# Performance work log

Measured on AMD Instinct MI355X. Metric: run time of the kernel, lower is better.

## Reference

```python
import jax, jax.numpy as jnp
import numpy as np

B, N, DIM = 8, 8192, 256
HEADS, LOCAL_HEADS, WINDOW = 8, 1, 64
HD = DIM // HEADS  # 32
MLP_HIDDEN = 1024
EPS = 1e-5


def layer_norm(x, g, b):
    mu = jnp.mean(x, axis=-1, keepdims=True)
    var = jnp.var(x, axis=-1, keepdims=True)
    return (x - mu) * jax.lax.rsqrt(var + EPS) * g + b


def look_around(t, pad_value=0.0):
    # t: (b, nw, w, ...); concat windows [i-1, i, i+1] -> (b, nw, 3w, ...)
    nw = t.shape[1]
    pads = [(0, 0), (1, 1)] + [(0, 0)] * (t.ndim - 2)
    p = jnp.pad(t, pads, constant_values=pad_value)
    return jnp.concatenate([p[:, i:i + nw] for i in range(3)], axis=2)


def local_attn(q, k, v):
    # lucidrains LocalAttention, causal=False, look_backward=look_forward=1
    # q,k,v: (b_merged, n, d)
    b, n, d = q.shape
    nw = n // WINDOW
    scale = d ** -0.5
    bq = q.reshape(b, nw, WINDOW, d) * scale
    bk = look_around(k.reshape(b, nw, WINDOW, d))  # (b, nw, 3w, d)
    bv = look_around(v.reshape(b, nw, WINDOW, d))
    ticker = jnp.arange(n).reshape(1, nw, WINDOW)
    bq_k = look_around(ticker, pad_value=-1)       # (1, nw, 3w)
    pad_mask = (bq_k == -1)[:, :, None, :]         # (1, nw, 1, 3w)
    dots = jnp.einsum('bnie,bnje->bnij', bq, bk)   # (b, nw, w, 3w)
    dots = jnp.where(pad_mask, -1e9, dots)
    attn = jax.nn.softmax(dots, axis=-1)
    out = jnp.einsum('bnij,bnje->bnie', attn, bv)
    return out.reshape(b, n, d)


def linear_attn(q, k, v):
    # q,k,v: (b, h, n, d)
    d = q.shape[-1]
    qs = jax.nn.softmax(q, axis=-1) * d ** -0.5
    ks = jax.nn.softmax(k, axis=-2)
    ctx = jnp.einsum('bhnd,bhne->bhde', ks, v)     # (b, h, d, d) tiny
    return jnp.einsum('bhnd,bhde->bhne', qs, ctx)


def setup_inputs() -> dict:
    key = jax.random.key(0)
    ks = jax.random.split(key, 8)
    s = 0.02
    return {
        'x': jax.random.normal(ks[0], (B, N, DIM), jnp.float32),
        'norm1_g': jnp.ones((DIM,), jnp.float32),
        'norm1_b': jnp.zeros((DIM,), jnp.float32),
        'Wq': jax.random.normal(ks[1], (DIM, DIM), jnp.float32) * s,
        'Wkv': jax.random.normal(ks[2], (DIM, DIM), jnp.float32) * s,
        'Wproj': jax.random.normal(ks[3], (DIM, DIM), jnp.float32) * s,
        'bproj': jnp.zeros((DIM,), jnp.float32),
        'norm2_g': jnp.ones((DIM,), jnp.float32),
        'norm2_b': jnp.zeros((DIM,), jnp.float32),
        'W1': jax.random.normal(ks[4], (MLP_HIDDEN, DIM), jnp.float32) * s,
        'b1': jnp.zeros((MLP_HIDDEN,), jnp.float32),
        'W2': jax.random.normal(ks[5], (DIM, MLP_HIDDEN), jnp.float32) * s,
        'b2': jnp.zeros((DIM,), jnp.float32),
    }


def reference(x, norm1_g, norm1_b, Wq, Wkv, Wproj, bproj, norm2_g, norm2_b, W1, b1, W2, b2):
    b, n, c = x.shape
    h = layer_norm(x, norm1_g, norm1_b)
    q = h @ Wq.T
    kv = h @ Wkv.T  # k and v share the same projection in the original code
    split_heads = lambda t: t.reshape(b, n, HEADS, HD).transpose(0, 2, 1, 3)
    q, k, v = split_heads(q), split_heads(kv), split_heads(kv)
    lq, gq = q[:, :LOCAL_HEADS], q[:, LOCAL_HEADS:]
    lk, gk = k[:, :LOCAL_HEADS], k[:, LOCAL_HEADS:]
    lv, gv = v[:, :LOCAL_HEADS], v[:, LOCAL_HEADS:]
    lout = local_attn(lq.reshape(b * LOCAL_HEADS, n, HD),
                      lk.reshape(b * LOCAL_HEADS, n, HD),
                      lv.reshape(b * LOCAL_HEADS, n, HD)).reshape(b, LOCAL_HEADS, n, HD)
    gout = linear_attn(gq, gk, gv)
    attn = jnp.concatenate([lout, gout], axis=1)   # (b, H, n, hd)
    y = attn.transpose(0, 2, 1, 3).reshape(b, n, c) @ Wproj.T + bproj
    x = x + y
    h2 = layer_norm(x, norm2_g, norm2_b)
    m = jax.nn.gelu(h2 @ W1.T + b1, approximate=False) @ W2.T + b2
    return x + m
```

## Files before the change

### kernel.cpp

```cpp
#include <hip/hip_runtime.h>
#include <hip/hip_bf16.h>

typedef __bf16 bf16;
typedef __bf16 bf16x8 __attribute__((ext_vector_type(8)));
typedef float f32x4 __attribute__((ext_vector_type(4)));

__device__ __forceinline__ void gld16(const void* g, void* l) {
  __builtin_amdgcn_global_load_lds((const __attribute__((address_space(1))) void*)g,
                                   (__attribute__((address_space(3))) void*)l, 16, 0, 0);
}

__global__ void cvt_weights(const float* __restrict__ wq, const float* __restrict__ wkv,
                            const float* __restrict__ wp, const float* __restrict__ w1,
                            const float* __restrict__ w2,
                            bf16* __restrict__ wqkv, bf16* __restrict__ wpb,
                            bf16* __restrict__ w1b, bf16* __restrict__ w2b) {
  int i = blockIdx.x * 256 + threadIdx.x;
  if (i < 65536) wqkv[i] = (bf16)wq[i];
  else if (i < 131072) wqkv[i] = (bf16)wkv[i - 65536];
  else if (i < 196608) wpb[i - 131072] = (bf16)wp[i - 131072];
  else if (i < 458752) w1b[i - 196608] = (bf16)w1[i - 196608];
  else if (i < 720896) w2b[i - 458752] = (bf16)w2[i - 458752];
}

__launch_bounds__(256)
__global__ void ln_kernel(const float* __restrict__ x, const float* __restrict__ g,
                          const float* __restrict__ b, bf16* __restrict__ out) {
  const int row = blockIdx.x * 4 + (threadIdx.x >> 6);
  const int lane = threadIdx.x & 63;
  const float4 v = ((const float4*)(x + (long)row * 256))[lane];
  float s = v.x + v.y + v.z + v.w;
#pragma unroll
  for (int o = 1; o < 64; o <<= 1) s += __shfl_xor(s, o);
  const float mu = s * (1.f / 256.f);
  const float dx = v.x - mu, dy = v.y - mu, dz = v.z - mu, dw = v.w - mu;
  float q = dx * dx + dy * dy + dz * dz + dw * dw;
#pragma unroll
  for (int o = 1; o < 64; o <<= 1) q += __shfl_xor(q, o);
  const float rstd = rsqrtf(q * (1.f / 256.f) + 1e-5f);
  const float4 gg = ((const float4*)g)[lane];
  const float4 bb = ((const float4*)b)[lane];
  union { bf16 h[4]; uint2 u; } pk;
  pk.h[0] = (bf16)(dx * rstd * gg.x + bb.x);
  pk.h[1] = (bf16)(dy * rstd * gg.y + bb.y);
  pk.h[2] = (bf16)(dz * rstd * gg.z + bb.z);
  pk.h[3] = (bf16)(dw * rstd * gg.w + bb.w);
  *(uint2*)(out + (long)row * 256 + lane * 4) = pk.u;
}

template <int EPI, int NCG, int NCHUNK, int THREADS, int MSPLIT>
__launch_bounds__(THREADS, 4)
__global__ void gemm_pb(const bf16* __restrict__ A, const bf16* __restrict__ Bw,
                        void* C, const float* __restrict__ bias,
                        const float* res, int ldC) {
  constexpr int WAVES = THREADS / 64;
  constexpr int WR = 2;
  constexpr int WC = WAVES / WR;
  constexpr int FN = 2;
  constexpr int FM = 64 / WR / 16;
  constexpr int COLS = WC * FN * 16;
  constexpr int KK = NCHUNK * 128;
  constexpr int ITER = 64 * 128 * 2 / (THREADS * 16);
  constexpr int TILES = 65536 / MSPLIT / 64;
  constexpr int CHB = 64 * 128 * 2;
  constexpr int BSZ = (EPI == 1) ? 64 * COLS * 4 : 64 * COLS * 2;
  constexpr int NST = (EPI == 1) ? 12 : 2;
  constexpr int NBLK = NCG * MSPLIT;
  __shared__ char smem[3 * CHB + BSZ];
  const int tid = threadIdx.x;
  const int w = tid >> 6, lane = tid & 63;
  const int l15 = lane & 15, l4 = lane >> 4;
  const int wrow = w & (WR - 1), wcol = w / WR;
  const int bid = blockIdx.x;
  const int slot = (bid & 7) * (NBLK / 8) + (bid >> 3);
  const int cg = slot % NCG;
  const long strip0 = (long)(slot / NCG) * (65536 / MSPLIT);

  const bf16* Bl = Bw + (long)(cg * COLS + wcol * FN * 16 + l15) * KK + l4 * 8;
  bf16x8 Breg[NCHUNK][4][FN];
#pragma unroll
  for (int c = 0; c < NCHUNK; ++c)
#pragma unroll
    for (int kl = 0; kl < 4; ++kl)
#pragma unroll
      for (int fn = 0; fn < FN; ++fn)
        Breg[c][kl][fn] = *(const bf16x8*)(Bl + (long)fn * 16 * KK + c * 128 + kl * 32);

  float bias_r[FN];
  if constexpr (EPI == 2) {
#pragma unroll
    for (int fn = 0; fn < FN; ++fn)
      bias_r[fn] = bias[cg * COLS + wcol * FN * 16 + fn * 16 + l15];
  }
  asm volatile("" ::: "memory");

  auto stage = [&](int m, int c, int buf) {
#pragma unroll
    for (int it = 0; it < ITER; ++it) {
      const int p = it * (THREADS * 16) + tid * 16;
      const int row = p >> 8;
      const int colb = (p & 255) ^ ((row & 7) << 4);
      gld16((const char*)A + ((strip0 + m * 64 + row) * KK + c * 128) * 2 + colb,
            smem + buf * CHB + it * (THREADS * 16) + w * 1024);
    }
  };

  f32x4 acc[FM][FN] = {};
  stage(0, 0, 0);
  stage(0, 1, 1);

  for (int m = 0; m < TILES; ++m) {
#pragma unroll
    for (int c = 0; c < NCHUNK; ++c) {
      const int s = m * NCHUNK + c;
      if (m == 0 || c >= 2) {
        asm volatile("s_waitcnt vmcnt(%0)" ::"i"(ITER) : "memory");
      } else {
        asm volatile("s_waitcnt vmcnt(%0)" ::"i"(ITER + NST) : "memory");
      }
      __syncthreads();
      {
        int c2 = c + 2, m2 = m;
        if (c2 >= NCHUNK) { c2 -= NCHUNK; ++m2; }
        if (m2 < TILES) stage(m2, c2, (s + 2) % 3);
      }
      const char* Ab = smem + (s % 3) * CHB;
#pragma unroll
      for (int kl = 0; kl < 4; ++kl) {
        bf16x8 af[FM];
#pragma unroll
        for (int fm = 0; fm < FM; ++fm) {
          const int arow = wrow * (64 / WR) + fm * 16 + l15;
          af[fm] = *(const bf16x8*)(Ab + arow * 256 + ((kl * 64 + l4 * 16) ^ ((l15 & 7) << 4)));
        }
#pragma unroll
        for (int fm = 0; fm < FM; ++fm)
#pragma unroll
          for (int fn = 0; fn < FN; ++fn)
            acc[fm][fn] = __builtin_amdgcn_mfma_f32_16x16x32_bf16(af[fm], Breg[c][kl][fn],
                                                                  acc[fm][fn], 0, 0, 0);
      }
      if (c == NCHUNK - 1) {
        if constexpr (EPI == 1) {
          float* fb = (float*)(smem + 3 * CHB);
#pragma unroll
          for (int fm = 0; fm < FM; ++fm)
#pragma unroll
            for (int fn = 0; fn < FN; ++fn)
#pragma unroll
              for (int r = 0; r < 4; ++r)
                fb[(wrow * (64 / WR) + fm * 16 + l4 * 4 + r) * COLS +
                   wcol * FN * 16 + fn * 16 + l15] = acc[fm][fn][r];
          __syncthreads();
#pragma unroll
          for (int it = 0; it < 64 * COLS * 4 / (THREADS * 16); ++it) {
            const int off = it * (THREADS * 16) + tid * 16;
            const int row = off / (COLS * 4);
            const int colb = off % (COLS * 4);
            const long gb = ((strip0 + m * 64 + row) * ldC + cg * COLS) * 4 + colb;
            float4 v = *(const float4*)(smem + 3 * CHB + off);
            const float4 rr = *(const float4*)((const char*)res + gb);
            const float4 bv = *(const float4*)((const char*)bias + cg * COLS * 4 + colb);
            v.x += rr.x + bv.x; v.y += rr.y + bv.y;
            v.z += rr.z + bv.z; v.w += rr.w + bv.w;
            *(float4*)((char*)C + gb) = v;
          }
        } else {
          bf16* bb = (bf16*)(smem + 3 * CHB);
#pragma unroll
          for (int fm = 0; fm < FM; ++fm)
#pragma unroll
            for (int fn = 0; fn < FN; ++fn)
#pragma unroll
              for (int r = 0; r < 4; ++r) {
                float v = acc[fm][fn][r];
                if constexpr (EPI == 2) {
                  v += bias_r[fn];
                  v = 0.5f * v * (1.f + erff(v * 0.70710678118654752f));
                }
                bb[(wrow * (64 / WR) + fm * 16 + l4 * 4 + r) * COLS +
                   wcol * FN * 16 + fn * 16 + l15] = (bf16)v;
              }
          __syncthreads();
#pragma unroll
          for (int it = 0; it < 64 * COLS * 2 / (THREADS * 16); ++it) {
            const int off = it * (THREADS * 16) + tid * 16;
            const int row = off / (COLS * 2);
            const int colb = off % (COLS * 2);
            *(uint4*)((char*)C + ((strip0 + m * 64 + row) * ldC + cg * COLS) * 2 + colb) =
                *(const uint4*)(smem + 3 * CHB + off);
          }
        }
#pragma unroll
        for (int fm = 0; fm < FM; ++fm)
#pragma unroll
          for (int fn = 0; fn < FN; ++fn)
            acc[fm][fn] = f32x4{0.f, 0.f, 0.f, 0.f};
      }
    }
  }
}

__launch_bounds__(256, 3)
__global__ void gemm_mlp2(const bf16* __restrict__ A, const bf16* __restrict__ Bw,
                          float* __restrict__ C, const float* __restrict__ bias) {
  constexpr int TILES = 2, NCHUNK = 8, ITER = 4, CHB = 64 * 128 * 2;
  __shared__ char smem[3 * CHB];
  const int tid = threadIdx.x;
  const int w = tid >> 6, lane = tid & 63;
  const int l15 = lane & 15, l4 = lane >> 4;
  const int bid = blockIdx.x;
  const int slot = (bid & 7) * 128 + (bid >> 3);
  const int cg = slot & 1;
  const long strip0 = (long)(slot >> 1) * 128;
  const bf16* Bl = Bw + (long)(cg * 128 + w * 32 + l15) * 1024 + l4 * 8;
  const float bias0 = bias[cg * 128 + w * 32 + l15];
  const float bias1 = bias[cg * 128 + w * 32 + 16 + l15];

  auto stage = [&](int m, int c, int buf) {
#pragma unroll
    for (int it = 0; it < ITER; ++it) {
      const int p = it * 4096 + tid * 16;
      const int row = p >> 8;
      const int colb = (p & 255) ^ ((row & 7) << 4);
      gld16((const char*)A + ((strip0 + m * 64 + row) * 1024 + c * 128) * 2 + colb,
            smem + buf * CHB + it * 4096 + w * 1024);
    }
  };
  auto loadB = [&](int c, bf16x8 (&Bn)[2][4]) {
#pragma unroll
    for (int fn = 0; fn < 2; ++fn)
#pragma unroll
      for (int kl = 0; kl < 4; ++kl)
        Bn[fn][kl] = *(const bf16x8*)(Bl + (long)fn * 16 * 1024 + c * 128 + kl * 32);
  };

  bf16x8 B0[2][4], B1[2][4];
  f32x4 acc[4][2] = {};
  stage(0, 0, 0);
  stage(0, 1, 1);
  loadB(0, B0);

  auto body = [&](int m, int c, bf16x8 (&Bu)[2][4], bf16x8 (&Bn)[2][4]) {
    const int s = m * NCHUNK + c;
    if (s == 0)
      asm volatile("s_waitcnt vmcnt(12)" ::: "memory");
    else if (s == TILES * NCHUNK - 1)
      asm volatile("s_waitcnt vmcnt(16)" ::: "memory");
    else
      asm volatile("s_waitcnt vmcnt(20)" ::: "memory");
    __syncthreads();
    {
      int c2 = c + 2, m2 = m;
      if (c2 >= NCHUNK) { c2 -= NCHUNK; ++m2; }
      if (m2 < TILES) stage(m2, c2, (s + 2) % 3);
    }
    loadB((c + 1) & 7, Bn);
    const char* Ab = smem + (s % 3) * CHB;
#pragma unroll
    for (int kl = 0; kl < 4; ++kl) {
      bf16x8 af[4];
#pragma unroll
      for (int fm = 0; fm < 4; ++fm)
        af[fm] = *(const bf16x8*)(Ab + (fm * 16 + l15) * 256 + ((kl * 64 + l4 * 16) ^ ((l15 & 7) << 4)));
#pragma unroll
      for (int fm = 0; fm < 4; ++fm) {
        acc[fm][0] = __builtin_amdgcn_mfma_f32_16x16x32_bf16(af[fm], Bu[0][kl], acc[fm][0], 0, 0, 0);
        acc[fm][1] = __builtin_amdgcn_mfma_f32_16x16x32_bf16(af[fm], Bu[1][kl], acc[fm][1], 0, 0, 0);
      }
    }
    if (c == NCHUNK - 1) {
#pragma unroll
      for (int fm = 0; fm < 4; ++fm)
#pragma unroll
        for (int r = 0; r < 4; ++r) {
          const long row = strip0 + m * 64 + fm * 16 + l4 * 4 + r;
          const long i0 = row * 256 + cg * 128 + w * 32 + l15;
          C[i0]      = acc[fm][0][r] + bias0 + C[i0];
          C[i0 + 16] = acc[fm][1][r] + bias1 + C[i0 + 16];
          acc[fm][0][r] = 0.f;
          acc[fm][1][r] = 0.f;
        }
      asm volatile("s_waitcnt vmcnt(12)" ::: "memory");
    }
  };

  for (int m = 0; m < TILES; ++m) {
#pragma unroll
    for (int cp = 0; cp < NCHUNK; cp += 2) {
      body(m, cp, B0, B1);
      body(m, cp + 1, B1, B0);
    }
  }
}

__launch_bounds__(256)
__global__ void lattn_kernel(const bf16* __restrict__ qkv, bf16* __restrict__ attn) {
  const int j = blockIdx.x, b = blockIdx.y;
  const int tid = threadIdx.x, w = tid >> 6, lane = tid & 63;
  __shared__ bf16 Qs[64 * 40];
  __shared__ bf16 Ks[192 * 40];
  __shared__ bf16 Kt[32 * 200];
  __shared__ bf16 Ps[4][16 * 200];
  const float scale = 0.17677669529663687f;
  const long base = (long)b * 8192 + (long)j * 64;
  for (int i = tid; i < 64 * 32; i += 256) {
    const int r = i >> 5, d = i & 31;
    Qs[r * 40 + d] = (bf16)((float)qkv[(base + r) * 512 + d] * scale);
  }
  for (int i = tid; i < 192 * 32; i += 256) {
    const int c = i >> 5, d = i & 31;
    const long tc = (long)j * 64 - 64 + c;
    float kv = 0.f;
    if (tc >= 0 && tc < 8192) kv = (float)qkv[((long)b * 8192 + tc) * 512 + 256 + d];
    const bf16 kb = (bf16)kv;
    Ks[c * 40 + d] = kb;
    Kt[d * 200 + c] = kb;
  }
  __syncthreads();
  const int l15 = lane & 15, l4 = lane >> 4;
  const bf16x8 aq = *(const bf16x8*)(Qs + (w * 16 + l15) * 40 + l4 * 8);
  const f32x4 zz = {0.f, 0.f, 0.f, 0.f};
  f32x4 S[12];
#pragma unroll
  for (int fn = 0; fn < 12; ++fn) {
    const bf16x8 bk = *(const bf16x8*)(Ks + (fn * 16 + l15) * 40 + l4 * 8);
    S[fn] = __builtin_amdgcn_mfma_f32_16x16x32_bf16(aq, bk, zz, 0, 0, 0);
  }
#pragma unroll
  for (int fn = 0; fn < 12; ++fn) {
    const long tc = (long)j * 64 - 64 + fn * 16 + l15;
    if (tc < 0 || tc >= 8192) { S[fn][0] = -1e9f; S[fn][1] = -1e9f; S[fn][2] = -1e9f; S[fn][3] = -1e9f; }
  }
  float sinv[4];
#pragma unroll
  for (int r = 0; r < 4; ++r) {
    float m = -1e30f;
#pragma unroll
    for (int fn = 0; fn < 12; ++fn) m = fmaxf(m, S[fn][r]);
#pragma unroll
    for (int o = 1; o < 16; o <<= 1) m = fmaxf(m, __shfl_xor(m, o));
    float s = 0.f;
#pragma unroll
    for (int fn = 0; fn < 12; ++fn) { const float e = __expf(S[fn][r] - m); S[fn][r] = e; s += e; }
#pragma unroll
    for (int o = 1; o < 16; o <<= 1) s += __shfl_xor(s, o);
    sinv[r] = 1.f / s;
  }
#pragma unroll
  for (int fn = 0; fn < 12; ++fn)
#pragma unroll
    for (int r = 0; r < 4; ++r)
      Ps[w][(l4 * 4 + r) * 200 + fn * 16 + l15] = (bf16)(S[fn][r] * sinv[r]);
  __syncthreads();
  f32x4 O[2] = {};
#pragma unroll
  for (int ks = 0; ks < 6; ++ks) {
    const bf16x8 ap = *(const bf16x8*)(Ps[w] + l15 * 200 + ks * 32 + l4 * 8);
#pragma unroll
    for (int fe = 0; fe < 2; ++fe) {
      const bf16x8 bv = *(const bf16x8*)(Kt + (fe * 16 + l15) * 200 + ks * 32 + l4 * 8);
      O[fe] = __builtin_amdgcn_mfma_f32_16x16x32_bf16(ap, bv, O[fe], 0, 0, 0);
    }
  }
#pragma unroll
  for (int fe = 0; fe < 2; ++fe)
#pragma unroll
    for (int r = 0; r < 4; ++r)
      attn[(base + w * 16 + l4 * 4 + r) * 256 + fe * 16 + l15] = (bf16)O[fe][r];
}

__launch_bounds__(256)
__global__ void ctx_kernel(const bf16* __restrict__ qkv, float* __restrict__ ctx,
                           float* __restrict__ S) {
  const int bh = blockIdx.x;
  const int b = bh / 7, h = bh % 7 + 1;
  const int tid = threadIdx.x;
  const int w = tid >> 6, lane = tid & 63;
  const int l15 = lane & 15, l4 = lane >> 4;
  __shared__ bf16 evT[32 * 264];
  __shared__ bf16 kT[48 * 264];
  __shared__ float red[4][32 * 48];
  const long n0 = (long)blockIdx.y * 256;
  const bf16* kp = qkv + ((long)b * 8192 + n0 + tid) * 512 + 256 + h * 32;
  bf16x8 kv[4];
#pragma unroll
  for (int c = 0; c < 4; ++c) kv[c] = *(const bf16x8*)(kp + c * 8);
#pragma unroll
  for (int i = 0; i < 16; ++i)
    kT[(32 + i) * 264 + tid] = (i == 0) ? (bf16)1.0f : (bf16)0.0f;
#pragma unroll
  for (int c = 0; c < 4; ++c)
#pragma unroll
    for (int j = 0; j < 8; ++j) {
      const int d = c * 8 + j;
      evT[d * 264 + tid] = (bf16)__expf((float)kv[c][j]);
      kT[d * 264 + tid] = kv[c][j];
    }
  __syncthreads();
  f32x4 acc[2][3] = {};
#pragma unroll
  for (int ks = 0; ks < 2; ++ks) {
    const int ncol = w * 64 + ks * 32 + l4 * 8;
    bf16x8 af[2], bb[3];
#pragma unroll
    for (int fm = 0; fm < 2; ++fm) af[fm] = *(const bf16x8*)(evT + (fm * 16 + l15) * 264 + ncol);
#pragma unroll
    for (int fe = 0; fe < 3; ++fe) bb[fe] = *(const bf16x8*)(kT + (fe * 16 + l15) * 264 + ncol);
#pragma unroll
    for (int fm = 0; fm < 2; ++fm)
#pragma unroll
      for (int fe = 0; fe < 3; ++fe)
        acc[fm][fe] = __builtin_amdgcn_mfma_f32_16x16x32_bf16(af[fm], bb[fe], acc[fm][fe], 0, 0, 0);
  }
#pragma unroll
  for (int fm = 0; fm < 2; ++fm)
#pragma unroll
    for (int fe = 0; fe < 3; ++fe)
#pragma unroll
      for (int r = 0; r < 4; ++r)
        red[w][(fm * 16 + l4 * 4 + r) * 48 + fe * 16 + l15] = acc[fm][fe][r];
  __syncthreads();
  for (int i = tid; i < 32 * 48; i += 256) {
    const float v = red[0][i] + red[1][i] + red[2][i] + red[3][i];
    const int d = i / 48, e = i - d * 48;
    if (e < 32) atomicAdd(ctx + (long)bh * 1024 + d * 32 + e, v);
    else if (e == 32) atomicAdd(S + bh * 32 + d, v);
  }
}

__launch_bounds__(256)
__global__ void lout_kernel(const bf16* __restrict__ qkv, const float* __restrict__ S,
                            const float* __restrict__ ctx, bf16* __restrict__ attn) {
  const int bh = blockIdx.x;
  const int b = bh / 7, h = bh % 7 + 1;
  const int tid = threadIdx.x;
  const int w = tid >> 6, lane = tid & 63;
  const int l15 = lane & 15, l4 = lane >> 4;
  __shared__ bf16 qs[256 * 40];
  __shared__ bf16 C2t[32 * 40];
  const long n0 = (long)blockIdx.y * 256;
  for (int i = tid; i < 1024; i += 256) {
    const int e = i >> 5, d = i & 31;
    C2t[e * 40 + d] = (bf16)(ctx[(long)bh * 1024 + d * 32 + e] / S[bh * 32 + d]);
  }
  const bf16* qp = qkv + ((long)b * 8192 + n0 + tid) * 512 + h * 32;
  bf16x8 qv[4];
#pragma unroll
  for (int c = 0; c < 4; ++c) qv[c] = *(const bf16x8*)(qp + c * 8);
  float qf[32];
#pragma unroll
  for (int c = 0; c < 4; ++c)
#pragma unroll
    for (int j = 0; j < 8; ++j) qf[c * 8 + j] = (float)qv[c][j];
  float m = qf[0];
#pragma unroll
  for (int d = 1; d < 32; ++d) m = fmaxf(m, qf[d]);
  float s = 0.f;
#pragma unroll
  for (int d = 0; d < 32; ++d) { qf[d] = __expf(qf[d] - m); s += qf[d]; }
  const float f = 0.17677669529663687f / s;
#pragma unroll
  for (int c = 0; c < 4; ++c) {
    bf16x8 o;
#pragma unroll
    for (int j = 0; j < 8; ++j) o[j] = (bf16)(qf[c * 8 + j] * f);
    *(bf16x8*)(qs + tid * 40 + c * 8) = o;
  }
  __syncthreads();
  f32x4 acc[4][2] = {};
  bf16x8 bfr[2];
#pragma unroll
  for (int fe = 0; fe < 2; ++fe) bfr[fe] = *(const bf16x8*)(C2t + (fe * 16 + l15) * 40 + l4 * 8);
#pragma unroll
  for (int fm = 0; fm < 4; ++fm) {
    const bf16x8 af = *(const bf16x8*)(qs + (w * 64 + fm * 16 + l15) * 40 + l4 * 8);
#pragma unroll
    for (int fe = 0; fe < 2; ++fe)
      acc[fm][fe] = __builtin_amdgcn_mfma_f32_16x16x32_bf16(af, bfr[fe], acc[fm][fe], 0, 0, 0);
  }
#pragma unroll
  for (int fm = 0; fm < 4; ++fm)
#pragma unroll
    for (int fe = 0; fe < 2; ++fe)
#pragma unroll
      for (int r = 0; r < 4; ++r)
        attn[((long)b * 8192 + n0 + w * 64 + fm * 16 + l4 * 4 + r) * 256 + h * 32 + fe * 16 + l15]
            = (bf16)acc[fm][fe][r];
}

extern "C" void kernel_launch(void* const* d_in, const int* in_sizes, int n_in,
                              void* d_out, int out_size, void* d_ws, size_t ws_size,
                              hipStream_t stream) {
  const float* x     = (const float*)d_in[0];
  const float* n1g   = (const float*)d_in[1];
  const float* n1b   = (const float*)d_in[2];
  const float* Wq    = (const float*)d_in[3];
  const float* Wkv   = (const float*)d_in[4];
  const float* Wproj = (const float*)d_in[5];
  const float* bproj = (const float*)d_in[6];
  const float* n2g   = (const float*)d_in[7];
  const float* n2b   = (const float*)d_in[8];
  const float* W1    = (const float*)d_in[9];
  const float* b1    = (const float*)d_in[10];
  const float* W2    = (const float*)d_in[11];
  const float* b2    = (const float*)d_in[12];
  float* out = (float*)d_out;
  char* ws = (char*)d_ws;

  bf16* wqkv   = (bf16*)(ws + 0);
  bf16* wprojb = (bf16*)(ws + 262144);
  bf16* w1b    = (bf16*)(ws + 393216);
  bf16* w2b    = (bf16*)(ws + 917504);
  float* Sbuf  = (float*)(ws + 1441792);
  float* ctx   = (float*)(ws + 1448960);
  bf16* hbuf   = (bf16*)(ws + 1685504);
  bf16* qkv    = (bf16*)(ws + 35239936);
  bf16* hidden = qkv;

  cvt_weights<<<2816, 256, 0, stream>>>(Wq, Wkv, Wproj, W1, W2, wqkv, wprojb, w1b, w2b);
  ln_kernel<<<16384, 256, 0, stream>>>(x, n1g, n1b, hbuf);
  gemm_pb<0, 4, 2, 512, 128><<<512, 512, 0, stream>>>(hbuf, wqkv, qkv, nullptr, nullptr, 512);
  hipMemsetAsync(Sbuf, 0, 7168 + 229376, stream);
  lattn_kernel<<<dim3(128, 8), 256, 0, stream>>>(qkv, hbuf);
  ctx_kernel<<<dim3(56, 32), 256, 0, stream>>>(qkv, ctx, Sbuf);
  lout_kernel<<<dim3(56, 32), 256, 0, stream>>>(qkv, Sbuf, ctx, hbuf);
  gemm_pb<1, 2, 2, 512, 256><<<512, 512, 0, stream>>>(hbuf, wprojb, out, bproj, x, 256);
  ln_kernel<<<16384, 256, 0, stream>>>(out, n2g, n2b, hbuf);
  gemm_pb<2, 8, 2, 512, 64><<<512, 512, 0, stream>>>(hbuf, w1b, hidden, b1, nullptr, 1024);
  gemm_mlp2<<<1024, 256, 0, stream>>>(hidden, w2b, out, b2);
}
```

Before: 355.2 us.

## Split-K the MLP down-projection GEMM with register-resident weights and atomic accumulation

The second MLP GEMM now splits the K=1024 reduction into two halves across blockIdx.y. Each block uses 512 threads (8 waves in a 2x4 layout) and keeps its whole B-weight slice for its K half in registers, loaded once up front. This replaces the per-chunk double-buffered B loads. Partial results are added into the residual output with atomicAdd, and the bias is added only by the first K half. The change adds more parallelism and removes repeated weight loads, at the cost of float atomics on the output, higher register pressure, and a reduction order that is no longer deterministic.

```diff
diff --git a/kernel.cpp b/kernel.cpp
--- a/kernel.cpp
+++ b/kernel.cpp
@@ -201,95 +201,95 @@
   }
 }
 
-__launch_bounds__(256, 3)
+__launch_bounds__(512, 2)
 __global__ void gemm_mlp2(const bf16* __restrict__ A, const bf16* __restrict__ Bw,
                           float* __restrict__ C, const float* __restrict__ bias) {
-  constexpr int TILES = 2, NCHUNK = 8, ITER = 4, CHB = 64 * 128 * 2;
+  constexpr int ITER = 2, NCHUNK = 4, TILES = 4, CHB = 64 * 128 * 2;
   __shared__ char smem[3 * CHB];
   const int tid = threadIdx.x;
   const int w = tid >> 6, lane = tid & 63;
   const int l15 = lane & 15, l4 = lane >> 4;
+  const int wrow = w & 1, wcol = w >> 1;
+  const int kh = blockIdx.y;
   const int bid = blockIdx.x;
-  const int slot = (bid & 7) * 128 + (bid >> 3);
+  const int slot = (bid & 7) * 64 + (bid >> 3);
   const int cg = slot & 1;
-  const long strip0 = (long)(slot >> 1) * 128;
-  const bf16* Bl = Bw + (long)(cg * 128 + w * 32 + l15) * 1024 + l4 * 8;
-  const float bias0 = bias[cg * 128 + w * 32 + l15];
-  const float bias1 = bias[cg * 128 + w * 32 + 16 + l15];
+  const long strip0 = (long)(slot >> 1) * 256;
+
+  const bf16* Bl = Bw + (long)(cg * 128 + wcol * 32 + l15) * 1024 + kh * 512 + l4 * 8;
+  bf16x8 Breg[NCHUNK][4][2];
+#pragma unroll
+  for (int c = 0; c < NCHUNK; ++c)
+#pragma unroll
+    for (int kl = 0; kl < 4; ++kl)
+#pragma unroll
+      for (int fn = 0; fn < 2; ++fn)
+        Breg[c][kl][fn] = *(const bf16x8*)(Bl + (long)fn * 16 * 1024 + c * 128 + kl * 32);
+  float biasr[2];
+#pragma unroll
+  for (int fn = 0; fn < 2; ++fn)
+    biasr[fn] = kh ? 0.f : bias[cg * 128 + wcol * 32 + fn * 16 + l15];
+  asm volatile("" ::: "memory");
 
   auto stage = [&](int m, int c, int buf) {
 #pragma unroll
     for (int it = 0; it < ITER; ++it) {
-      const int p = it * 4096 + tid * 16;
+      const int p = it * 8192 + tid * 16;
       const int row = p >> 8;
       const int colb = (p & 255) ^ ((row & 7) << 4);
-      gld16((const char*)A + ((strip0 + m * 64 + row) * 1024 + c * 128) * 2 + colb,
-            smem + buf * CHB + it * 4096 + w * 1024);
+      gld16((const char*)A + (((strip0 + m * 64 + row) * 1024) + kh * 512 + c * 128) * 2 + colb,
+            smem + buf * CHB + it * 8192 + w * 1024);
     }
   };
-  auto loadB = [&](int c, bf16x8 (&Bn)[2][4]) {
-#pragma unroll
-    for (int fn = 0; fn < 2; ++fn)
-#pragma unroll
-      for (int kl = 0; kl < 4; ++kl)
-        Bn[fn][kl] = *(const bf16x8*)(Bl + (long)fn * 16 * 1024 + c * 128 + kl * 32);
-  };
-
-  bf16x8 B0[2][4], B1[2][4];
-  f32x4 acc[4][2] = {};
+
+  f32x4 acc[2][2] = {};
   stage(0, 0, 0);
   stage(0, 1, 1);
-  loadB(0, B0);
-
-  auto body = [&](int m, int c, bf16x8 (&Bu)[2][4], bf16x8 (&Bn)[2][4]) {
-    const int s = m * NCHUNK + c;
-    if (s == 0)
-      asm volatile("s_waitcnt vmcnt(12)" ::: "memory");
-    else if (s == TILES * NCHUNK - 1)
-      asm volatile("s_waitcnt vmcnt(16)" ::: "memory");
-    else
-      asm volatile("s_waitcnt vmcnt(20)" ::: "memory");
-    __syncthreads();
-    {
-      int c2 = c + 2, m2 = m;
-      if (c2 >= NCHUNK) { c2 -= NCHUNK; ++m2; }
-      if (m2 < TILES) stage(m2, c2, (s + 2) % 3);
-    }
-    loadB((c + 1) & 7, Bn);
-    const char* Ab = smem + (s % 3) * CHB;
-#pragma unroll
-    for (int kl = 0; kl < 4; ++kl) {
-      bf16x8 af[4];
-#pragma unroll
-      for (int fm = 0; fm < 4; ++fm)
-        af[fm] = *(const bf16x8*)(Ab + (fm * 16 + l15) * 256 + ((kl * 64 + l4 * 16) ^ ((l15 & 7) << 4)));
-#pragma unroll
-      for (int fm = 0; fm < 4; ++fm) {
-        acc[fm][0] = __builtin_amdgcn_mfma_f32_16x16x32_bf16(af[fm], Bu[0][kl], acc[fm][0], 0, 0, 0);
-        acc[fm][1] = __builtin_amdgcn_mfma_f32_16x16x32_bf16(af[fm], Bu[1][kl], acc[fm][1], 0, 0, 0);
-      }
-    }
-    if (c == NCHUNK - 1) {
-#pragma unroll
-      for (int fm = 0; fm < 4; ++fm)
-#pragma unroll
-        for (int r = 0; r < 4; ++r) {
-          const long row = strip0 + m * 64 + fm * 16 + l4 * 4 + r;
-          const long i0 = row * 256 + cg * 128 + w * 32 + l15;
-          C[i0]      = acc[fm][0][r] + bias0 + C[i0];
-          C[i0 + 16] = acc[fm][1][r] + bias1 + C[i0 + 16];
-          acc[fm][0][r] = 0.f;
-          acc[fm][1][r] = 0.f;
+
+  for (int m = 0; m < TILES; ++m) {
+#pragma unroll
+    for (int c = 0; c < NCHUNK; ++c) {
+      const int s = m * NCHUNK + c;
+      if (m == 0 || c >= 2) {
+        asm volatile("s_waitcnt vmcnt(2)" ::: "memory");
+      } else {
+        asm volatile("s_waitcnt vmcnt(18)" ::: "memory");
+      }
+      __syncthreads();
+      {
+        int c2 = c + 2, m2 = m;
+        if (c2 >= NCHUNK) { c2 -= NCHUNK; ++m2; }
+        if (m2 < TILES) stage(m2, c2, (s + 2) % 3);
+      }
+      const char* Ab = smem + (s % 3) * CHB;
+#pragma unroll
+      for (int kl = 0; kl < 4; ++kl) {
+        bf16x8 af[2];
+#pragma unroll
+        for (int fm = 0; fm < 2; ++fm) {
+          const int arow = wrow * 32 + fm * 16 + l15;
+          af[fm] = *(const bf16x8*)(Ab + arow * 256 + ((kl * 64 + l4 * 16) ^ ((l15 & 7) << 4)));
         }
-      asm volatile("s_waitcnt vmcnt(12)" ::: "memory");
-    }
-  };
-
-  for (int m = 0; m < TILES; ++m) {
-#pragma unroll
-    for (int cp = 0; cp < NCHUNK; cp += 2) {
-      body(m, cp, B0, B1);
-      body(m, cp + 1, B1, B0);
+#pragma unroll
+        for (int fm = 0; fm < 2; ++fm)
+#pragma unroll
+          for (int fn = 0; fn < 2; ++fn)
+            acc[fm][fn] = __builtin_amdgcn_mfma_f32_16x16x32_bf16(af[fm], Breg[c][kl][fn],
+                                                                  acc[fm][fn], 0, 0, 0);
+      }
+      if (c == NCHUNK - 1) {
+#pragma unroll
+        for (int fm = 0; fm < 2; ++fm)
+#pragma unroll
+          for (int fn = 0; fn < 2; ++fn)
+#pragma unroll
+            for (int r = 0; r < 4; ++r) {
+              const long row = strip0 + m * 64 + wrow * 32 + fm * 16 + l4 * 4 + r;
+              const long idx = row * 256 + cg * 128 + wcol * 32 + fn * 16 + l15;
+              atomicAdd(&C[idx], acc[fm][fn][r] + biasr[fn]);
+              acc[fm][fn][r] = 0.f;
+            }
+      }
     }
   }
 }
@@ -528,5 +528,5 @@
   gemm_pb<1, 2, 2, 512, 256><<<512, 512, 0, stream>>>(hbuf, wprojb, out, bproj, x, 256);
   ln_kernel<<<16384, 256, 0, stream>>>(out, n2g, n2b, hbuf);
   gemm_pb<2, 8, 2, 512, 64><<<512, 512, 0, stream>>>(hbuf, w1b, hidden, b1, nullptr, 1024);
-  gemm_mlp2<<<1024, 256, 0, stream>>>(hidden, w2b, out, b2);
-}
+  gemm_mlp2<<<dim3(512, 2), 512, 0, stream>>>(hidden, w2b, out, b2);
+}
```

Result: slower. 374.4 us (+5.4%).
